# Performance work log

Hardware: AMD Instinct MI355X
Metric: run time of the kernel (lower is better)

## Reference

```python
import jax, jax.numpy as jnp
import numpy as np

B, C_IN, H, W = 16, 16, 64, 64
C_OUT, KH, KW, DH, DW = 16, 3, 3, 1, 1
OH = (H - KH) // DH + 1  # 62
OW = (W - KW) // DW + 1  # 62


def setup_inputs() -> dict:
    key = jax.random.key(0)
    k1, k2 = jax.random.split(key)
    x = jax.random.normal(k1, (B, C_IN, H, W), dtype=jnp.float32)
    weight = jax.random.normal(k2, (1, C_OUT, C_IN, OH, OW, KH * KW), dtype=jnp.float32)
    return {"x": x, "weight": weight}


def _extract_patches(x):
    # Equivalent to torch unfold(2,kh,dh).unfold(3,kw,dw).view(..., kh*kw):
    # patches[b,c,y,x,k] with k = i*KW + j (row-major over kernel window).
    slabs = [x[:, :, i:i + OH * DH:DH, j:j + OW * DW:DW]
             for i in range(KH) for j in range(KW)]
    return jnp.stack(slabs, axis=-1)  # [B, C_IN, OH, OW, KH*KW]


def reference(x, weight):
    patches = _extract_patches(x)
    # out[b,o,y,x] = sum_{c,k} patches[b,c,y,x,k] * weight[0,o,c,y,x,k]
    out = jnp.einsum('bcyxk,ocyxk->boyx', patches, weight[0])
    return out
```

## Files before the change

### kernel.cpp

```cpp
#include <hip/hip_runtime.h>


#define CIN   16
#define COUT  16
#define H_    64
#define W_    64
#define OH_   62
#define OW_   62
#define NB    16
#define TO    8

__global__ __launch_bounds__(256, 2)
void lc2d_kernel(const float* __restrict__ x,
                 const float* __restrict__ w,
                 float* __restrict__ out) {
    const int tid = threadIdx.x;
    const int xc  = tid & 15;
    const int b   = tid >> 4;
    const int x0  = blockIdx.x * 16;
    const int y   = blockIdx.y;
    const int o0  = blockIdx.z * TO;

    const int  xpos  = x0 + xc;
    const bool valid = (xpos < OW_);
    const int  xp    = valid ? xpos : (OW_ - 1);

    float acc[TO];
    #pragma unroll
    for (int t = 0; t < TO; ++t) acc[t] = 0.f;

    const float* xb = x + (size_t)b * (CIN * H_ * W_) + (size_t)y * W_ + xp;
    const size_t WOSTR = (size_t)CIN * OH_ * OW_ * 9;
    const size_t WCSTR = (size_t)OH_ * OW_ * 9;
    const float* wb = w + (size_t)o0 * WOSTR + ((size_t)y * OW_ + xp) * 9;

    for (int c = 0; c < CIN; ++c) {
        const float* xr = xb + (size_t)c * (H_ * W_);
        const float* wc = wb + (size_t)c * WCSTR;

        float xv[9];
        #pragma unroll
        for (int i = 0; i < 3; ++i)
            #pragma unroll
            for (int j = 0; j < 3; ++j)
                xv[i * 3 + j] = xr[i * W_ + j];

        #pragma unroll
        for (int k = 0; k < 9; ++k) {
            #pragma unroll
            for (int t = 0; t < TO; ++t) {
                acc[t] = fmaf(wc[(size_t)t * WOSTR + k], xv[k], acc[t]);
            }
        }
    }

    if (valid) {
        float* ob = out + (size_t)b * (COUT * OH_ * OW_)
                        + (size_t)o0 * (OH_ * OW_)
                        + (size_t)y * OW_ + xpos;
        #pragma unroll
        for (int t = 0; t < TO; ++t)
            ob[(size_t)t * (OH_ * OW_)] = acc[t];
    }
}

extern "C" void kernel_launch(void* const* d_in, const int* in_sizes, int n_in,
                              void* d_out, int out_size, void* d_ws, size_t ws_size,
                              hipStream_t stream) {
    const float* x = (const float*)d_in[0];
    const float* w = (const float*)d_in[1];
    float* out = (float*)d_out;

    dim3 grid(4, OH_, COUT / TO);
    dim3 block(256);
    lc2d_kernel<<<grid, block, 0, stream>>>(x, w, out);
}
```

Baseline: 107.2 us.

## Stage weights in LDS with coalesced float2 loads and register-blocked batch tiling

Each block now loads the weight slab for 8 output channels and 32 x-positions cooperatively with float2 loads, scatters it into a padded LDS layout, and prefetches the next channel's weights into registers while computing the current one. Each thread computes a 4x4 tile of output channels by batch, reading weights as float4 from LDS. The old version did strided per-thread global weight loads of 9 floats each. This trades extra LDS traffic and two barriers per input channel for coalesced global weight reads. The grid shrinks to 248 blocks at one block per SIMD-set, which lowers occupancy.

```diff
diff --git a/kernel.cpp b/kernel.cpp
--- a/kernel.cpp
+++ b/kernel.cpp
@@ -3,64 +3,159 @@
 
 #define CIN   16
 #define COUT  16
-#define H_    64
-#define W_    64
-#define OH_   62
-#define OW_   62
-#define NB    16
-#define TO    8
+#define HH    64
+#define WW    64
+#define OHH   62
+#define OWW   62
 
-__global__ __launch_bounds__(256, 2)
-void lc2d_kernel(const float* __restrict__ x,
-                 const float* __restrict__ w,
-                 float* __restrict__ out) {
+#define WOSTR (CIN * OHH * OWW * 9)
+#define WCSTR (OHH * OWW * 9)
+#define OROW  388
+
+__device__ __forceinline__ int ldsIdx(int o, int xi, int k) {
+    int j = k >> 2;
+    int p = (j + xi) % 3;
+    return o * OROW + xi * 12 + p * 4 + (k & 3);
+}
+
+__global__ __launch_bounds__(256, 1)
+void lc2d(const float* __restrict__ xg,
+          const float* __restrict__ wg,
+          float* __restrict__ outg)
+{
+    __shared__ float Wl[8 * OROW];
+
     const int tid = threadIdx.x;
-    const int xc  = tid & 15;
-    const int b   = tid >> 4;
-    const int x0  = blockIdx.x * 16;
-    const int y   = blockIdx.y;
-    const int o0  = blockIdx.z * TO;
+    const int y   = blockIdx.x;
+    const int xh  = blockIdx.y;
+    const int oh  = blockIdx.z;
+    const int x0  = xh * 32;
+    const int nx  = xh ? (OWW - 32) : 32;
+    const int M   = nx * 9 / 2;
+    const int tot = 8 * M;
 
-    const int  xpos  = x0 + xc;
-    const bool valid = (xpos < OW_);
-    const int  xp    = valid ? xpos : (OW_ - 1);
+    const int xl  = tid & 31;
+    const int og  = (tid >> 5) & 1;
+    const int bg  = tid >> 6;
+    const int pos = x0 + xl;
+    const bool valid = pos < OWW;
+    const int xp  = valid ? pos : (OWW - 1);
 
-    float acc[TO];
+    int st_o[5], st_fo[5];
+    bool st_en[5];
     #pragma unroll
-    for (int t = 0; t < TO; ++t) acc[t] = 0.f;
+    for (int r = 0; r < 5; ++r) {
+        int id = tid + 256 * r;
+        st_en[r] = id < tot;
+        int idc = st_en[r] ? id : 0;
+        int o = idc / M;
+        st_o[r]  = o;
+        st_fo[r] = 2 * (idc - o * M);
+    }
 
-    const float* xb = x + (size_t)b * (CIN * H_ * W_) + (size_t)y * W_ + xp;
-    const size_t WOSTR = (size_t)CIN * OH_ * OW_ * 9;
-    const size_t WCSTR = (size_t)OH_ * OW_ * 9;
-    const float* wb = w + (size_t)o0 * WOSTR + ((size_t)y * OW_ + xp) * 9;
+    const float* wbase = wg + (size_t)oh * 8 * WOSTR + (size_t)(y * OWW + x0) * 9;
+
+    float2 pf[5];
+    #pragma unroll
+    for (int r = 0; r < 5; ++r)
+        if (st_en[r])
+            pf[r] = *(const float2*)(wbase + (size_t)st_o[r] * WOSTR + st_fo[r]);
+    #pragma unroll
+    for (int r = 0; r < 5; ++r) {
+        if (st_en[r]) {
+            int fo = st_fo[r];
+            int xi = fo / 9;
+            int k  = fo - xi * 9;
+            Wl[ldsIdx(st_o[r], xi, k)] = pf[r].x;
+            int xi2 = (k == 8) ? xi + 1 : xi;
+            int k2  = (k == 8) ? 0 : k + 1;
+            Wl[ldsIdx(st_o[r], xi2, k2)] = pf[r].y;
+        }
+    }
+    __syncthreads();
+
+    float acc[4][4];
+    #pragma unroll
+    for (int t = 0; t < 4; ++t)
+        #pragma unroll
+        for (int b = 0; b < 4; ++b) acc[t][b] = 0.f;
+
+    const float* xbb = xg + (size_t)y * WW + xp;
 
     for (int c = 0; c < CIN; ++c) {
-        const float* xr = xb + (size_t)c * (H_ * W_);
-        const float* wc = wb + (size_t)c * WCSTR;
+        float2 npf[5];
+        if (c + 1 < CIN) {
+            #pragma unroll
+            for (int r = 0; r < 5; ++r)
+                if (st_en[r])
+                    npf[r] = *(const float2*)(wbase + (size_t)st_o[r] * WOSTR
+                                              + (size_t)(c + 1) * WCSTR + st_fo[r]);
+        }
 
-        float xv[9];
+        float xv[4][9];
         #pragma unroll
-        for (int i = 0; i < 3; ++i)
+        for (int b = 0; b < 4; ++b) {
+            const float* xr = xbb + (size_t)(bg * 4 + b) * (CIN * HH * WW)
+                                  + (size_t)c * (HH * WW);
             #pragma unroll
-            for (int j = 0; j < 3; ++j)
-                xv[i * 3 + j] = xr[i * W_ + j];
+            for (int i = 0; i < 3; ++i)
+                #pragma unroll
+                for (int j = 0; j < 3; ++j)
+                    xv[b][i * 3 + j] = xr[i * WW + j];
+        }
 
         #pragma unroll
-        for (int k = 0; k < 9; ++k) {
+        for (int t = 0; t < 4; ++t) {
+            const int lo   = og * 4 + t;
+            const int base = lo * OROW + xl * 12;
+            const int p0   = xl % 3;
+            const float4 w0 = *(const float4*)&Wl[base + p0 * 4];
+            const float4 w1 = *(const float4*)&Wl[base + ((p0 + 1) % 3) * 4];
+            const float  w8 = Wl[base + ((p0 + 2) % 3) * 4];
             #pragma unroll
-            for (int t = 0; t < TO; ++t) {
-                acc[t] = fmaf(wc[(size_t)t * WOSTR + k], xv[k], acc[t]);
+            for (int b = 0; b < 4; ++b) {
+                float s = acc[t][b];
+                s = fmaf(w0.x, xv[b][0], s);
+                s = fmaf(w0.y, xv[b][1], s);
+                s = fmaf(w0.z, xv[b][2], s);
+                s = fmaf(w0.w, xv[b][3], s);
+                s = fmaf(w1.x, xv[b][4], s);
+                s = fmaf(w1.y, xv[b][5], s);
+                s = fmaf(w1.z, xv[b][6], s);
+                s = fmaf(w1.w, xv[b][7], s);
+                s = fmaf(w8,   xv[b][8], s);
+                acc[t][b] = s;
             }
+        }
+
+        if (c + 1 < CIN) {
+            __syncthreads();
+            #pragma unroll
+            for (int r = 0; r < 5; ++r) {
+                if (st_en[r]) {
+                    int fo = st_fo[r];
+                    int xi = fo / 9;
+                    int k  = fo - xi * 9;
+                    Wl[ldsIdx(st_o[r], xi, k)] = npf[r].x;
+                    int xi2 = (k == 8) ? xi + 1 : xi;
+                    int k2  = (k == 8) ? 0 : k + 1;
+                    Wl[ldsIdx(st_o[r], xi2, k2)] = npf[r].y;
+                }
+            }
+            __syncthreads();
         }
     }
 
     if (valid) {
-        float* ob = out + (size_t)b * (COUT * OH_ * OW_)
-                        + (size_t)o0 * (OH_ * OW_)
-                        + (size_t)y * OW_ + xpos;
         #pragma unroll
-        for (int t = 0; t < TO; ++t)
-            ob[(size_t)t * (OH_ * OW_)] = acc[t];
+        for (int t = 0; t < 4; ++t) {
+            const int o = oh * 8 + og * 4 + t;
+            #pragma unroll
+            for (int b = 0; b < 4; ++b) {
+                const int bb = bg * 4 + b;
+                outg[((size_t)(bb * COUT + o) * OHH + y) * OWW + pos] = acc[t][b];
+            }
+        }
     }
 }
 
@@ -71,7 +166,7 @@
     const float* w = (const float*)d_in[1];
     float* out = (float*)d_out;
 
-    dim3 grid(4, OH_, COUT / TO);
+    dim3 grid(OHH, 2, 2);
     dim3 block(256);
-    lc2d_kernel<<<grid, block, 0, stream>>>(x, w, out);
+    lc2d<<<grid, block, 0, stream>>>(x, w, out);
 }
```

Measured after the change: 90.65 us. -15.4%, faster.
